# Optimization experiments

Hardware: AMD Instinct MI355X
Metric: run time of the kernel (lower is better)

The kernel has to match this reference:

```python
import jax, jax.numpy as jnp
import numpy as np

B, N, H, L, R, E = 8, 10000, 64, 4, 3, 200000
FP, NUM_CELLS = 2048, 100
LN_EPS = 1e-3  # Keras LayerNormalization default epsilon


def setup_inputs() -> dict:
    key = jax.random.key(0)
    ks = jax.random.split(key, 24)
    g = lambda k, shape, fan: (jax.random.uniform(k, shape, jnp.float32) * 2 - 1) * np.sqrt(6.0 / fan)
    inp = {
        'ctl_expr': jax.random.normal(ks[0], (B, N), jnp.float32),
        'drug_targets': jax.random.uniform(ks[1], (B, N), jnp.float32),
        'drug_fp': jax.random.uniform(ks[2], (B, FP), jnp.float32),
        'edge_weight': jax.random.uniform(ks[3], (R, E), jnp.float32),
        'cell_idx': jax.random.randint(ks[4], (B,), 0, NUM_CELLS, jnp.int32),
        'edge_index': jax.random.randint(ks[5], (R, 2, E), 0, N, jnp.int32),
        # parameters
        'W_se': g(ks[6], (1, H), 1 + H),
        'b_se': jnp.zeros((H,), jnp.float32),
        'cell_emb': jax.random.normal(ks[7], (NUM_CELLS, H), jnp.float32) * 0.05,
        'W_f1': g(ks[8], (FP, H), FP + H),
        'b_f1': jnp.zeros((H,), jnp.float32),
        'W_f2': g(ks[9], (H, 2 * H), 3 * H) * 0.1,
        'b_f2': jnp.zeros((2 * H,), jnp.float32),
        'Wself': jnp.stack([g(ks[10 + l], (H, H), 2 * H) for l in range(L)]),
        'Wrel': jnp.stack([jnp.stack([g(jax.random.fold_in(ks[14], l * R + r), (H, H), 2 * H) for r in range(R)]) for l in range(L)]),
        'ln_g': jnp.ones((L, H), jnp.float32),
        'ln_b': jnp.zeros((L, H), jnp.float32),
        'W_out': g(ks[15], (H, 1), H + 1),
        'b_out': jnp.zeros((1,), jnp.float32),
    }
    return inp


def reference(ctl_expr, drug_targets, drug_fp, edge_weight, cell_idx, edge_index,
              W_se, b_se, cell_emb, W_f1, b_f1, W_f2, b_f2,
              Wself, Wrel, ln_g, ln_b, W_out, b_out):
    # shared_embedding: Dense(H, relu) applied to scalar node features
    def shared(v):  # v: [B,N] -> [B,N,H]
        return jax.nn.relu(v[..., None] * W_se[0] + b_se)

    x = shared(ctl_expr) + shared(drug_targets)            # [B,N,H]
    x = x + cell_emb[cell_idx][:, None, :]                 # cell embedding broadcast

    # drug FiLM: gamma/beta conditioning
    film = jax.nn.relu(drug_fp @ W_f1 + b_f1) @ W_f2 + b_f2  # [B,2H]
    gamma, beta = jnp.split(film, 2, axis=-1)
    gamma = jnp.tanh(gamma)
    x = x * (1.0 + gamma[:, None, :]) + beta[:, None, :]

    n_layers, n_rel = Wself.shape[0], Wrel.shape[1]
    for l in range(n_layers):
        out = x @ Wself[l]                                 # self projection [B,N,H]
        for r in range(n_rel):
            src, dst = edge_index[r, 0], edge_index[r, 1]
            h = x @ Wrel[l, r]                             # [B,N,H]
            msg = edge_weight[r][None, :, None] * h[:, src, :]  # [B,E,H]
            out = out.at[:, dst].add(msg)                  # scatter-add to dst nodes
        # LayerNorm over feature dim (Keras eps=1e-3)
        mu = out.mean(-1, keepdims=True)
        var = ((out - mu) ** 2).mean(-1, keepdims=True)
        out = (out - mu) * jax.lax.rsqrt(var + LN_EPS) * ln_g[l] + ln_b[l]
        x = jax.nn.relu(out)

    return (x @ W_out)[..., 0] + b_out[0]                  # [B,N]
```

## Files before the change

### kernel.cpp

```cpp
#include <hip/hip_runtime.h>
#include <hip/hip_bf16.h>
#include <math.h>

#define Bk 8
#define Nk 10000
#define Hk 64
#define Lk 4
#define Rk 3
#define Ek 200000
#define FPk 2048

typedef unsigned short u16;
typedef unsigned int   u32;
typedef _Float16 f16;
typedef __attribute__((ext_vector_type(2))) _Float16 f16x2;
typedef __attribute__((ext_vector_type(8))) _Float16 f16x8;
typedef __attribute__((ext_vector_type(4))) float f32x4;

__device__ __forceinline__ f16x2 as_h2(u32 u){
    union{u32 i; f16x2 h;} v; v.i = u; return v.h;
}
__device__ __forceinline__ u32 as_u32(f16x2 h){
    union{u32 i; f16x2 h;} v; v.h = h; return v.i;
}
__device__ __forceinline__ u16 f2h_bits(float f){
    union{f16 h; u16 u;} v; v.h = (f16)f; return v.u;
}

__global__ void k_zero(int* p, int n){
    int i = blockIdx.x*256 + threadIdx.x;
    if(i < n) p[i] = 0;
}

__global__ void k_count(const int* edge_index, int* deg){
    int idx = blockIdx.x*256 + threadIdx.x;
    if(idx >= Rk*Ek) return;
    int r = idx / Ek, e = idx % Ek;
    int dst = edge_index[r*2*Ek + Ek + e];
    atomicAdd(&deg[r*Nk + dst], 1);
}

__global__ void k_scan(const int* deg, int* offs, int* cursor){
    int r = blockIdx.x;
    __shared__ int s[1024];
    int t = threadIdx.x;
    int base_i = t*10;
    int local[10];
    int sum = 0;
    if(base_i < Nk){
        #pragma unroll
        for(int k = 0; k < 10; ++k){ local[k] = deg[r*Nk + base_i + k]; sum += local[k]; }
    }
    s[t] = sum;
    __syncthreads();
    for(int d = 1; d < 1024; d <<= 1){
        int v = (t >= d) ? s[t-d] : 0;
        __syncthreads();
        s[t] += v;
        __syncthreads();
    }
    if(base_i < Nk){
        int excl = s[t] - sum;
        #pragma unroll
        for(int k = 0; k < 10; ++k){
            offs[r*(Nk+1) + base_i + k] = excl;
            cursor[r*Nk + base_i + k]   = excl;
            excl += local[k];
        }
    }
    if(t == 1023) offs[r*(Nk+1) + Nk] = s[1023];
}

__global__ void k_fill(const int* edge_index, const float* edge_weight,
                       int* cursor, int2* epack){
    int idx = blockIdx.x*256 + threadIdx.x;
    if(idx >= Rk*Ek) return;
    int r = idx / Ek, e = idx % Ek;
    int src = edge_index[r*2*Ek + e];
    int dst = edge_index[r*2*Ek + Ek + e];
    int pos = atomicAdd(&cursor[r*Nk + dst], 1);
    f16 h = (f16)edge_weight[r*Ek + e];
    epack[(size_t)r*Ek + pos] = make_int2(src << 7, (int)as_u32((f16x2){h, h}));
}

__global__ void k_wprep(const float* __restrict__ Wself, const float* __restrict__ Wrel,
                        u16* __restrict__ wt){
    int idx = blockIdx.x*256 + threadIdx.x;
    if(idx >= Lk*4*2*4*64*8) return;
    int j    = idx & 7;
    int lane = (idx >> 3) & 63;
    int jt   = (idx >> 9) & 3;
    int kc   = (idx >> 11) & 1;
    int mt   = (idx >> 12) & 3;
    int l    = idx >> 14;
    int k    = kc*32 + (lane >> 4)*8 + j;
    int col  = jt*16 + (lane & 15);
    float w = (mt == 0) ? Wself[(l*64 + k)*64 + col]
                        : Wrel[((l*3 + (mt-1))*64 + k)*64 + col];
    wt[idx] = f2h_bits(w);
}

__global__ void k_film1(const float* fp, const float* W1, const float* b1, float* hid){
    int b = blockIdx.x >> 6, h = blockIdx.x & 63;
    const float* fpb = fp + b*FPk;
    float acc = 0.f;
    for(int k = threadIdx.x; k < FPk; k += 256)
        acc += fpb[k] * W1[k*64 + h];
    __shared__ float red[256];
    red[threadIdx.x] = acc;
    __syncthreads();
    for(int s = 128; s >= 1; s >>= 1){
        if(threadIdx.x < s) red[threadIdx.x] += red[threadIdx.x + s];
        __syncthreads();
    }
    if(threadIdx.x == 0) hid[b*64 + h] = fmaxf(red[0] + b1[h], 0.f);
}

__global__ void k_film2(const float* hid, const float* W2, const float* b2,
                        float* g1p, float* beta){
    int b = blockIdx.x, j = threadIdx.x;
    float acc = b2[j];
    for(int k = 0; k < 64; ++k)
        acc += hid[b*64 + k] * W2[k*128 + j];
    if(j < 64) g1p[b*64 + j] = 1.f + tanhf(acc);
    else       beta[b*64 + j - 64] = acc;
}

__global__ void k_init(const float* ctl, const float* dt, const int* cell_idx,
                       const float* W_se, const float* b_se, const float* cell_emb,
                       const float* g1p, const float* beta, u16* xh){
    const size_t total = (size_t)Bk*Nk*64;
    for(size_t i = (size_t)blockIdx.x*256 + threadIdx.x; i < total; i += (size_t)gridDim.x*256){
        int h = (int)(i & 63);
        size_t bn = i >> 6;
        int b = (int)(bn / Nk);
        float w = W_se[h], bs = b_se[h];
        float v = fmaxf(ctl[bn]*w + bs, 0.f) + fmaxf(dt[bn]*w + bs, 0.f)
                + cell_emb[cell_idx[b]*64 + h];
        xh[i] = f2h_bits(v * g1p[b*64 + h] + beta[b*64 + h]);
    }
}

__global__ __launch_bounds__(256) void k_agg(const u16* __restrict__ xh,
                      const int* __restrict__ offs, const int2* __restrict__ epack,
                      u16* __restrict__ aggh){
    __shared__ int2 stash[4][64];
    int bpair = blockIdx.x & 3;
    int grp   = blockIdx.x >> 2;
    int wq    = threadIdx.x >> 6;
    int wid   = grp*4 + wq;
    int lane  = threadIdx.x & 63;
    int fg    = lane & 31;
    int bl    = lane >> 5;
    int b     = bpair*2 + bl;
    int r = wid / Nk, dst = wid % Nk;
    int o0 = offs[r*(Nk+1) + dst], o1 = offs[r*(Nk+1) + dst + 1];
    const int2* ep = epack + (size_t)r*Ek;
    const char* xb = (const char*)xh + (size_t)b*Nk*128 + fg*4;

    f16x2 A = (f16x2){0,0}, C = (f16x2){0,0};
    int2* st = stash[wq];
    for(int base = o0; base < o1; base += 64){
        int j = base + lane;
        if(j < o1) st[lane] = ep[j];
        int cnt = min(o1 - base, 64);
        int t = 0;
        for(; t + 8 <= cnt; t += 8){
            int4 q01 = *(const int4*)&st[t];
            int4 q23 = *(const int4*)&st[t+2];
            int4 q45 = *(const int4*)&st[t+4];
            int4 q67 = *(const int4*)&st[t+6];
            u32 u0 = *(const u32*)(xb + q01.x);
            u32 u1 = *(const u32*)(xb + q01.z);
            u32 u2 = *(const u32*)(xb + q23.x);
            u32 u3 = *(const u32*)(xb + q23.z);
            u32 u4 = *(const u32*)(xb + q45.x);
            u32 u5 = *(const u32*)(xb + q45.z);
            u32 u6 = *(const u32*)(xb + q67.x);
            u32 u7 = *(const u32*)(xb + q67.z);
            A += as_h2(u0)*as_h2(q01.y); C += as_h2(u1)*as_h2(q01.w);
            A += as_h2(u2)*as_h2(q23.y); C += as_h2(u3)*as_h2(q23.w);
            A += as_h2(u4)*as_h2(q45.y); C += as_h2(u5)*as_h2(q45.w);
            A += as_h2(u6)*as_h2(q67.y); C += as_h2(u7)*as_h2(q67.w);
        }
        for(; t + 2 <= cnt; t += 2){
            int4 q01 = *(const int4*)&st[t];
            u32 u0 = *(const u32*)(xb + q01.x);
            u32 u1 = *(const u32*)(xb + q01.z);
            A += as_h2(u0)*as_h2(q01.y); C += as_h2(u1)*as_h2(q01.w);
        }
        if(t < cnt){
            int2 p = st[t];
            u32 u = *(const u32*)(xb + p.x);
            A += as_h2(u)*as_h2(p.y);
        }
    }
    float a0 = (float)A.x + (float)C.x;
    float a1 = (float)A.y + (float)C.y;
    u32 packed = (u32)f2h_bits(a0) | ((u32)f2h_bits(a1) << 16);
    ((u32*)aggh)[(((size_t)r*Bk + b)*Nk + dst)*32 + fg] = packed;
}

__global__ __launch_bounds__(256) void k_proj_mfma(u16* __restrict__ xh,
        const u16* __restrict__ aggh, const u16* __restrict__ wt,
        const float* __restrict__ ln_g, const float* __restrict__ ln_b, int l,
        int last, const float* __restrict__ W_out, const float* __restrict__ b_out,
        float* __restrict__ out){
    int lane = threadIdx.x & 63;
    int wq   = threadIdx.x >> 6;
    int b    = blockIdx.y;
    int n0   = blockIdx.x*64 + wq*16;
    int mrow = lane & 15;
    int kq   = lane >> 4;
    int node_a = n0 + mrow;
    if(node_a >= Nk) node_a = Nk - 1;

    f32x4 acc[4];
    #pragma unroll
    for(int jt = 0; jt < 4; ++jt) acc[jt] = (f32x4){0.f,0.f,0.f,0.f};

    const u16* wl = wt + (size_t)l*16384;

    #pragma unroll
    for(int mt = 0; mt < 4; ++mt){
        const u16* arow = (mt == 0)
            ? xh   + ((size_t)b*Nk + node_a)*64
            : aggh + (((size_t)(mt-1)*Bk + b)*Nk + node_a)*64;
        #pragma unroll
        for(int kc = 0; kc < 2; ++kc){
            f16x8 afrag = *(const f16x8*)(arow + kc*32 + kq*8);
            #pragma unroll
            for(int jt = 0; jt < 4; ++jt){
                size_t wi = ((size_t)((mt*2 + kc)*4 + jt)*64 + lane)*8;
                f16x8 bfrag = *(const f16x8*)(wl + wi);
                acc[jt] = __builtin_amdgcn_mfma_f32_16x16x32_f16(afrag, bfrag, acc[jt], 0, 0, 0);
            }
        }
    }

    float gv[4], bv[4], wo[4];
    #pragma unroll
    for(int jt = 0; jt < 4; ++jt){
        int f = jt*16 + mrow;
        gv[jt] = ln_g[l*64 + f];
        bv[jt] = ln_b[l*64 + f];
        wo[jt] = W_out[f];
    }
    float bo = b_out[0];

    u16* xdst = xh + (size_t)b*Nk*64;
    #pragma unroll
    for(int v = 0; v < 4; ++v){
        float s1 = acc[0][v] + acc[1][v] + acc[2][v] + acc[3][v];
        float s2 = acc[0][v]*acc[0][v] + acc[1][v]*acc[1][v]
                 + acc[2][v]*acc[2][v] + acc[3][v]*acc[3][v];
        #pragma unroll
        for(int off = 1; off <= 8; off <<= 1){
            s1 += __shfl_xor(s1, off);
            s2 += __shfl_xor(s2, off);
        }
        float mu  = s1 * 0.015625f;
        float var = s2 * 0.015625f - mu*mu;
        float rstd = rsqrtf(var + 1e-3f);
        int node = n0 + kq*4 + v;
        if(!last){
            if(node < Nk){
                #pragma unroll
                for(int jt = 0; jt < 4; ++jt){
                    float o = (acc[jt][v] - mu) * rstd * gv[jt] + bv[jt];
                    xdst[(size_t)node*64 + jt*16 + mrow] = f2h_bits(fmaxf(o, 0.f));
                }
            }
        }else{
            float s3 = 0.f;
            #pragma unroll
            for(int jt = 0; jt < 4; ++jt){
                float o = (acc[jt][v] - mu) * rstd * gv[jt] + bv[jt];
                s3 += fmaxf(o, 0.f) * wo[jt];
            }
            #pragma unroll
            for(int off = 1; off <= 8; off <<= 1)
                s3 += __shfl_xor(s3, off);
            if(mrow == 0 && node < Nk)
                out[(size_t)b*Nk + node] = s3 + bo;
        }
    }
}

extern "C" void kernel_launch(void* const* d_in, const int* in_sizes, int n_in,
                              void* d_out, int out_size, void* d_ws, size_t ws_size,
                              hipStream_t stream){
    const float* ctl        = (const float*)d_in[0];
    const float* dt         = (const float*)d_in[1];
    const float* drug_fp    = (const float*)d_in[2];
    const float* edge_w     = (const float*)d_in[3];
    const int*   cell_idx   = (const int*)  d_in[4];
    const int*   edge_index = (const int*)  d_in[5];
    const float* W_se       = (const float*)d_in[6];
    const float* b_se       = (const float*)d_in[7];
    const float* cell_emb   = (const float*)d_in[8];
    const float* W_f1       = (const float*)d_in[9];
    const float* b_f1       = (const float*)d_in[10];
    const float* W_f2       = (const float*)d_in[11];
    const float* b_f2       = (const float*)d_in[12];
    const float* Wself      = (const float*)d_in[13];
    const float* Wrel       = (const float*)d_in[14];
    const float* ln_g       = (const float*)d_in[15];
    const float* ln_b       = (const float*)d_in[16];
    const float* W_out      = (const float*)d_in[17];
    const float* b_out      = (const float*)d_in[18];
    float* out = (float*)d_out;

    char* p = (char*)d_ws;
    auto alloc = [&](size_t bytes)->char*{
        char* r = p; p += (bytes + 255) & ~(size_t)255; return r;
    };
    int*   deg    = (int*)  alloc((size_t)Rk*Nk*4);
    int*   cursor = (int*)  alloc((size_t)Rk*Nk*4);
    int*   offs   = (int*)  alloc((size_t)Rk*(Nk+1)*4);
    int2*  epack  = (int2*) alloc((size_t)Rk*Ek*8);
    float* hid    = (float*)alloc((size_t)Bk*64*4);
    float* g1p    = (float*)alloc((size_t)Bk*64*4);
    float* beta   = (float*)alloc((size_t)Bk*64*4);
    u16*   xh     = (u16*)  alloc((size_t)Bk*Nk*64*2);
    u16*   aggh   = (u16*)  alloc((size_t)3*Bk*Nk*64*2);
    u16*   wt     = (u16*)  alloc((size_t)Lk*16384*2);

    k_zero<<<(Rk*Nk + 255)/256, 256, 0, stream>>>(deg, Rk*Nk);
    k_count<<<(Rk*Ek + 255)/256, 256, 0, stream>>>(edge_index, deg);
    k_scan<<<Rk, 1024, 0, stream>>>(deg, offs, cursor);
    k_fill<<<(Rk*Ek + 255)/256, 256, 0, stream>>>(edge_index, edge_w, cursor, epack);

    k_wprep<<<(Lk*4*2*4*64*8 + 255)/256, 256, 0, stream>>>(Wself, Wrel, wt);

    k_film1<<<Bk*64, 256, 0, stream>>>(drug_fp, W_f1, b_f1, hid);
    k_film2<<<Bk, 128, 0, stream>>>(hid, W_f2, b_f2, g1p, beta);

    k_init<<<2048, 256, 0, stream>>>(ctl, dt, cell_idx, W_se, b_se, cell_emb, g1p, beta, xh);

    for(int l = 0; l < Lk; ++l){
        k_agg<<<4*7500, 256, 0, stream>>>(xh, offs, epack, aggh);
        k_proj_mfma<<<dim3((Nk + 63)/64, Bk), 256, 0, stream>>>(
            xh, aggh, wt, ln_g, ln_b, l,
            (l == Lk-1) ? 1 : 0, W_out, b_out, out);
    }
}
```

Baseline: 422.8 us.

## Fuse neighbor aggregation into per-layer MFMA projection kernel with ping-pong buffers

Replaces the separate aggregation and projection kernels with one per-layer kernel. Each wave gathers its 16 destination nodes' messages for all three relations into shared memory, then feeds them directly to the MFMA projection and LayerNorm. This removes the global write and read of the large aggregation buffer, and uses double-buffered node features to avoid read/write hazards. It also folds degree zeroing into the weight-prep kernel to drop a launch. The trade-off is much less parallelism for the latency-bound gathers, with serial per-node loops per wave.

```diff
diff --git a/kernel.cpp b/kernel.cpp
--- a/kernel.cpp
+++ b/kernel.cpp
@@ -25,11 +25,6 @@
 }
 __device__ __forceinline__ u16 f2h_bits(float f){
     union{f16 h; u16 u;} v; v.h = (f16)f; return v.u;
-}
-
-__global__ void k_zero(int* p, int n){
-    int i = blockIdx.x*256 + threadIdx.x;
-    if(i < n) p[i] = 0;
 }
 
 __global__ void k_count(const int* edge_index, int* deg){
@@ -84,8 +79,9 @@
 }
 
 __global__ void k_wprep(const float* __restrict__ Wself, const float* __restrict__ Wrel,
-                        u16* __restrict__ wt){
+                        u16* __restrict__ wt, int* __restrict__ deg){
     int idx = blockIdx.x*256 + threadIdx.x;
+    if(idx < Rk*Nk) deg[idx] = 0;
     if(idx >= Lk*4*2*4*64*8) return;
     int j    = idx & 7;
     int lane = (idx >> 3) & 63;
@@ -141,75 +137,72 @@
     }
 }
 
-__global__ __launch_bounds__(256) void k_agg(const u16* __restrict__ xh,
-                      const int* __restrict__ offs, const int2* __restrict__ epack,
-                      u16* __restrict__ aggh){
-    __shared__ int2 stash[4][64];
-    int bpair = blockIdx.x & 3;
-    int grp   = blockIdx.x >> 2;
-    int wq    = threadIdx.x >> 6;
-    int wid   = grp*4 + wq;
-    int lane  = threadIdx.x & 63;
-    int fg    = lane & 31;
-    int bl    = lane >> 5;
-    int b     = bpair*2 + bl;
-    int r = wid / Nk, dst = wid % Nk;
-    int o0 = offs[r*(Nk+1) + dst], o1 = offs[r*(Nk+1) + dst + 1];
-    const int2* ep = epack + (size_t)r*Ek;
-    const char* xb = (const char*)xh + (size_t)b*Nk*128 + fg*4;
-
-    f16x2 A = (f16x2){0,0}, C = (f16x2){0,0};
-    int2* st = stash[wq];
-    for(int base = o0; base < o1; base += 64){
-        int j = base + lane;
-        if(j < o1) st[lane] = ep[j];
-        int cnt = min(o1 - base, 64);
-        int t = 0;
-        for(; t + 8 <= cnt; t += 8){
-            int4 q01 = *(const int4*)&st[t];
-            int4 q23 = *(const int4*)&st[t+2];
-            int4 q45 = *(const int4*)&st[t+4];
-            int4 q67 = *(const int4*)&st[t+6];
-            u32 u0 = *(const u32*)(xb + q01.x);
-            u32 u1 = *(const u32*)(xb + q01.z);
-            u32 u2 = *(const u32*)(xb + q23.x);
-            u32 u3 = *(const u32*)(xb + q23.z);
-            u32 u4 = *(const u32*)(xb + q45.x);
-            u32 u5 = *(const u32*)(xb + q45.z);
-            u32 u6 = *(const u32*)(xb + q67.x);
-            u32 u7 = *(const u32*)(xb + q67.z);
-            A += as_h2(u0)*as_h2(q01.y); C += as_h2(u1)*as_h2(q01.w);
-            A += as_h2(u2)*as_h2(q23.y); C += as_h2(u3)*as_h2(q23.w);
-            A += as_h2(u4)*as_h2(q45.y); C += as_h2(u5)*as_h2(q45.w);
-            A += as_h2(u6)*as_h2(q67.y); C += as_h2(u7)*as_h2(q67.w);
-        }
-        for(; t + 2 <= cnt; t += 2){
-            int4 q01 = *(const int4*)&st[t];
-            u32 u0 = *(const u32*)(xb + q01.x);
-            u32 u1 = *(const u32*)(xb + q01.z);
-            A += as_h2(u0)*as_h2(q01.y); C += as_h2(u1)*as_h2(q01.w);
-        }
-        if(t < cnt){
-            int2 p = st[t];
-            u32 u = *(const u32*)(xb + p.x);
-            A += as_h2(u)*as_h2(p.y);
-        }
-    }
-    float a0 = (float)A.x + (float)C.x;
-    float a1 = (float)A.y + (float)C.y;
-    u32 packed = (u32)f2h_bits(a0) | ((u32)f2h_bits(a1) << 16);
-    ((u32*)aggh)[(((size_t)r*Bk + b)*Nk + dst)*32 + fg] = packed;
-}
-
-__global__ __launch_bounds__(256) void k_proj_mfma(u16* __restrict__ xh,
-        const u16* __restrict__ aggh, const u16* __restrict__ wt,
+__global__ __launch_bounds__(256) void k_layer(const u16* __restrict__ xin,
+        u16* __restrict__ xout,
+        const int* __restrict__ offs, const int2* __restrict__ epack,
+        const u16* __restrict__ wt,
         const float* __restrict__ ln_g, const float* __restrict__ ln_b, int l,
         int last, const float* __restrict__ W_out, const float* __restrict__ b_out,
         float* __restrict__ out){
+    __shared__ u32  aggt[4][3*16*36];
+    __shared__ int2 stash[4][64];
+
     int lane = threadIdx.x & 63;
     int wq   = threadIdx.x >> 6;
-    int b    = blockIdx.y;
-    int n0   = blockIdx.x*64 + wq*16;
+    int b    = blockIdx.x & 7;
+    int tile = blockIdx.x >> 3;
+    int n0   = tile*64 + wq*16;
+
+    int half = lane >> 5;
+    int fg   = lane & 31;
+    const char* xb = (const char*)xin + (size_t)b*Nk*128 + fg*4;
+
+    u32*  wavet = aggt[wq];
+    int2* st    = stash[wq];
+
+    for(int dl = 0; dl < 16; ++dl){
+        int dst = n0 + dl;
+        #pragma unroll
+        for(int r = 0; r < 3; ++r){
+            f16x2 A = (f16x2){0,0};
+            if(dst < Nk){
+                int o0 = offs[r*(Nk+1) + dst], o1 = offs[r*(Nk+1) + dst + 1];
+                const int2* ep = epack + (size_t)r*Ek;
+                for(int base = o0; base < o1; base += 64){
+                    int j = base + lane;
+                    st[lane] = (j < o1) ? ep[j] : make_int2(0, 0);
+                    int cnt = min(o1 - base, 64);
+                    int nIter = (cnt + 1) >> 1;
+                    int i = 0;
+                    for(; i + 4 <= nIter; i += 4){
+                        int2 r0 = st[2*(i+0) + half];
+                        int2 r1 = st[2*(i+1) + half];
+                        int2 r2 = st[2*(i+2) + half];
+                        int2 r3 = st[2*(i+3) + half];
+                        u32 u0 = *(const u32*)(xb + r0.x);
+                        u32 u1 = *(const u32*)(xb + r1.x);
+                        u32 u2 = *(const u32*)(xb + r2.x);
+                        u32 u3 = *(const u32*)(xb + r3.x);
+                        A += as_h2(u0)*as_h2(r0.y);
+                        A += as_h2(u1)*as_h2(r1.y);
+                        A += as_h2(u2)*as_h2(r2.y);
+                        A += as_h2(u3)*as_h2(r3.y);
+                    }
+                    for(; i < nIter; ++i){
+                        int2 rr = st[2*i + half];
+                        u32 u = *(const u32*)(xb + rr.x);
+                        A += as_h2(u)*as_h2(rr.y);
+                    }
+                }
+            }
+            u32 av = __shfl_xor(as_u32(A), 32);
+            float lo = (float)A.x + (float)as_h2(av).x;
+            float hi = (float)A.y + (float)as_h2(av).y;
+            if(half == 0)
+                wavet[(r*16 + dl)*36 + fg] = (u32)f2h_bits(lo) | ((u32)f2h_bits(hi) << 16);
+        }
+    }
+
     int mrow = lane & 15;
     int kq   = lane >> 4;
     int node_a = n0 + mrow;
@@ -220,15 +213,18 @@
     for(int jt = 0; jt < 4; ++jt) acc[jt] = (f32x4){0.f,0.f,0.f,0.f};
 
     const u16* wl = wt + (size_t)l*16384;
+    const u16* arow = xin + ((size_t)b*Nk + node_a)*64;
 
     #pragma unroll
     for(int mt = 0; mt < 4; ++mt){
-        const u16* arow = (mt == 0)
-            ? xh   + ((size_t)b*Nk + node_a)*64
-            : aggh + (((size_t)(mt-1)*Bk + b)*Nk + node_a)*64;
         #pragma unroll
         for(int kc = 0; kc < 2; ++kc){
-            f16x8 afrag = *(const f16x8*)(arow + kc*32 + kq*8);
+            f16x8 afrag;
+            if(mt == 0)
+                afrag = *(const f16x8*)(arow + kc*32 + kq*8);
+            else
+                afrag = *(const f16x8*)((const char*)wavet
+                         + ((((mt-1)*16 + mrow)*36 + kc*16 + kq*4) << 2));
             #pragma unroll
             for(int jt = 0; jt < 4; ++jt){
                 size_t wi = ((size_t)((mt*2 + kc)*4 + jt)*64 + lane)*8;
@@ -248,7 +244,7 @@
     }
     float bo = b_out[0];
 
-    u16* xdst = xh + (size_t)b*Nk*64;
+    u16* xdst = xout + (size_t)b*Nk*64;
     #pragma unroll
     for(int v = 0; v < 4; ++v){
         float s1 = acc[0][v] + acc[1][v] + acc[2][v] + acc[3][v];
@@ -322,26 +318,28 @@
     float* hid    = (float*)alloc((size_t)Bk*64*4);
     float* g1p    = (float*)alloc((size_t)Bk*64*4);
     float* beta   = (float*)alloc((size_t)Bk*64*4);
-    u16*   xh     = (u16*)  alloc((size_t)Bk*Nk*64*2);
-    u16*   aggh   = (u16*)  alloc((size_t)3*Bk*Nk*64*2);
+    u16*   xh_a   = (u16*)  alloc((size_t)Bk*Nk*64*2);
+    u16*   xh_b   = (u16*)  alloc((size_t)Bk*Nk*64*2);
     u16*   wt     = (u16*)  alloc((size_t)Lk*16384*2);
 
-    k_zero<<<(Rk*Nk + 255)/256, 256, 0, stream>>>(deg, Rk*Nk);
+    k_wprep<<<(Lk*4*2*4*64*8 + 255)/256, 256, 0, stream>>>(Wself, Wrel, wt, deg);
+
     k_count<<<(Rk*Ek + 255)/256, 256, 0, stream>>>(edge_index, deg);
     k_scan<<<Rk, 1024, 0, stream>>>(deg, offs, cursor);
     k_fill<<<(Rk*Ek + 255)/256, 256, 0, stream>>>(edge_index, edge_w, cursor, epack);
 
-    k_wprep<<<(Lk*4*2*4*64*8 + 255)/256, 256, 0, stream>>>(Wself, Wrel, wt);
-
     k_film1<<<Bk*64, 256, 0, stream>>>(drug_fp, W_f1, b_f1, hid);
     k_film2<<<Bk, 128, 0, stream>>>(hid, W_f2, b_f2, g1p, beta);
 
-    k_init<<<2048, 256, 0, stream>>>(ctl, dt, cell_idx, W_se, b_se, cell_emb, g1p, beta, xh);
-
+    k_init<<<2048, 256, 0, stream>>>(ctl, dt, cell_idx, W_se, b_se, cell_emb, g1p, beta, xh_a);
+
+    const int ntile = (Nk + 63)/64;
+    u16* xin   = xh_a;
+    u16* xout2 = xh_b;
     for(int l = 0; l < Lk; ++l){
-        k_agg<<<4*7500, 256, 0, stream>>>(xh, offs, epack, aggh);
-        k_proj_mfma<<<dim3((Nk + 63)/64, Bk), 256, 0, stream>>>(
-            xh, aggh, wt, ln_g, ln_b, l,
+        k_layer<<<ntile*8, 256, 0, stream>>>(
+            xin, xout2, offs, epack, wt, ln_g, ln_b, l,
             (l == Lk-1) ? 1 : 0, W_out, b_out, out);
-    }
-}
+        u16* tmp = xin; xin = xout2; xout2 = tmp;
+    }
+}
```

New measurement: 583.2 us. 1.38x slower.
